# Performance work log

Hardware: AMD Instinct MI355X
Metric: run time of the kernel (lower is better)

## Reference

```python
import jax, jax.numpy as jnp
import numpy as np

N, E = 50000, 800000
IN_DIM, HIDDEN, LATENT = 128, 256, 64


def setup_inputs() -> dict:
    key = jax.random.key(0)
    ks = jax.random.split(key, 10)
    def lin(k, fan_in, fan_out):
        s = 1.0 / np.sqrt(fan_in)
        return jax.random.uniform(k, (fan_in, fan_out), jnp.float32, -s, s)
    x = jax.random.normal(ks[0], (N, IN_DIM), jnp.float32)
    edge_index = jax.random.randint(ks[1], (2, E), 0, N, jnp.int64)
    return {
        "x": x,
        "edge_index": edge_index,
        # enc1: SAGEConv(in_dim, hidden): lin_l (neighbors, with bias), lin_r (root, no bias)
        "W1l": lin(ks[2], IN_DIM, HIDDEN),
        "b1": jnp.zeros((HIDDEN,), jnp.float32),
        "W1r": lin(ks[3], IN_DIM, HIDDEN),
        # enc2: SAGEConv(hidden, latent)
        "W2l": lin(ks[4], HIDDEN, LATENT),
        "b2": jnp.zeros((LATENT,), jnp.float32),
        "W2r": lin(ks[5], HIDDEN, LATENT),
        # decoder Linear(latent, in_dim)
        "Wd": lin(ks[6], LATENT, IN_DIM),
        "bd": jax.random.uniform(ks[7], (IN_DIM,), jnp.float32, -1.0 / np.sqrt(LATENT), 1.0 / np.sqrt(LATENT)),
    }


def _sage_conv(x, src, dst, Wl, b, Wr, num_nodes):
    # PyG SAGEConv (aggr='mean'): out = lin_l(mean_{j in N(i)} x_j) + lin_r(x_i)
    summed = jax.ops.segment_sum(x[src], dst, num_segments=num_nodes)   # [N, d]
    cnt = jax.ops.segment_sum(jnp.ones((src.shape[0],), x.dtype), dst, num_segments=num_nodes)
    mean = summed / jnp.maximum(cnt, 1.0)[:, None]
    return mean @ Wl + b + x @ Wr


def reference(x, edge_index, W1l, b1, W1r, W2l, b2, W2r, Wd, bd):
    src, dst = edge_index[0], edge_index[1]
    n = x.shape[0]
    h = jax.nn.relu(_sage_conv(x, src, dst, W1l, b1, W1r, n))
    z = _sage_conv(h, src, dst, W2l, b2, W2r, n)
    x_hat = z @ Wd + bd
    return (z, x_hat)
```

## Files before the change

kernel.cpp:

```cpp
#include <hip/hip_runtime.h>
#include <stdint.h>

#define NN 50000
#define NE 800000
#define NB 196
#define NBK 196
#define NBUK 196
#define CHK 4096
#define MTOT (NBUK * NBK)
#define MSB 151
#define CVTB 6250
#define PREPB 418

typedef __bf16 bf16x8 __attribute__((ext_vector_type(8)));
typedef float f32x4 __attribute__((ext_vector_type(4)));
typedef unsigned short ushort_t;

__device__ inline float bf2f(uint16_t u) {
    union { uint32_t i; float f; } v; v.i = ((uint32_t)u) << 16; return v.f;
}
__device__ inline uint16_t f2bf(float f) {
    uint32_t u = __float_as_uint(f);
    u += 0x7fffu + ((u >> 16) & 1u);
    return (uint16_t)(u >> 16);
}
__device__ inline float rdf(const void* p, int i, int bf) {
    return bf ? bf2f(((const ushort_t*)p)[i]) : ((const float*)p)[i];
}

__device__ inline int blk_or(int v, int* flag) {
    if (threadIdx.x == 0) *flag = 0;
    __syncthreads();
    if (v) atomicOr(flag, 1);
    __syncthreads();
    return *flag;
}
__device__ inline int detect_sh(const int* __restrict__ ei, int* flag) {
    int t = threadIdx.x;
    int v = ei[2 * t + 1] | ei[2 * (t + 256) + 1] | ei[2 * (t + 512) + 1] | ei[2 * (t + 768) + 1];
    return blk_or(v, flag) ? 0 : 1;
}
__device__ inline int detect_bf(const ushort_t* __restrict__ xw, int* flag) {
    int t = threadIdx.x;
    int bad = 0;
#pragma unroll
    for (int r = 0; r < 2; ++r) {
        uint16_t w = xw[t + 256 * r];
        int e = (w >> 7) & 0xFF;
        if (!(w == 0 || (e >= 96 && e <= 144))) bad = 1;
    }
    return blk_or(bad, flag) ? 0 : 1;
}

__global__ __launch_bounds__(256) void k_stage1(const int* __restrict__ ei, const void* __restrict__ x,
                                                const void* __restrict__ W1l, const void* __restrict__ W1r,
                                                const void* __restrict__ W2l, const void* __restrict__ W2r,
                                                const void* __restrict__ Wd,
                                                const void* __restrict__ b1, const void* __restrict__ b2,
                                                const void* __restrict__ bd,
                                                int* __restrict__ cntm, ushort_t* __restrict__ xb,
                                                ushort_t* __restrict__ wt, ushort_t* __restrict__ w2lt,
                                                ushort_t* __restrict__ w2rt, ushort_t* __restrict__ wdt,
                                                float* __restrict__ b1f, float* __restrict__ b2f,
                                                float* __restrict__ bdf) {
    __shared__ int flag;
    int b = blockIdx.x, t = threadIdx.x;
    if (b < NBK) {
        int sh = detect_sh(ei, &flag);
        __shared__ int hist[NBUK];
        if (t < NBUK) hist[t] = 0;
        __syncthreads();
        for (int i = t; i < CHK; i += 256) {
            int e = b * CHK + i;
            if (e < NE) {
                int d = ei[(size_t)(NE + e) << sh];
                atomicAdd(&hist[d >> 8], 1);
            }
        }
        __syncthreads();
        if (t < NBUK) cntm[t * NBK + b] = hist[t];
    } else if (b < NBK + CVTB) {
        int bf = detect_bf((const ushort_t*)x, &flag);
        int i = (b - NBK) * 256 + t;
        if (bf) {
            reinterpret_cast<ushort4*>(xb)[i] = reinterpret_cast<const ushort4*>(x)[i];
        } else {
            float4 v = reinterpret_cast<const float4*>(x)[i];
            ushort4 o;
            o.x = f2bf(v.x); o.y = f2bf(v.y); o.z = f2bf(v.z); o.w = f2bf(v.w);
            reinterpret_cast<ushort4*>(xb)[i] = o;
        }
    } else {
        int bf = detect_bf((const ushort_t*)x, &flag);
        int idx = (b - NBK - CVTB) * 256 + t;
        if (idx < 65536) {
            int c = idx >> 8, k = idx & 255;
            float v = (k < 128) ? rdf(W1l, k * 256 + c, bf) : rdf(W1r, (k - 128) * 256 + c, bf);
            wt[c * 256 + k] = f2bf(v);
        } else if (idx < 81920) {
            int t2 = idx - 65536;
            int c = t2 >> 8, k = t2 & 255;
            w2lt[c * 256 + k] = f2bf(rdf(W2l, k * 64 + c, bf));
        } else if (idx < 98304) {
            int t2 = idx - 81920;
            int c = t2 >> 8, k = t2 & 255;
            w2rt[c * 256 + k] = f2bf(rdf(W2r, k * 64 + c, bf));
        } else if (idx < 106496) {
            int t2 = idx - 98304;
            int c = t2 >> 6, k = t2 & 63;
            wdt[c * 64 + k] = f2bf(rdf(Wd, k * 128 + c, bf));
        } else if (idx < 106752) {
            b1f[idx - 106496] = rdf(b1, idx - 106496, bf);
        } else if (idx < 106816) {
            b2f[idx - 106752] = rdf(b2, idx - 106752, bf);
        } else if (idx < 106944) {
            bdf[idx - 106816] = rdf(bd, idx - 106816, bf);
        }
    }
}

__device__ inline int block_scan256(int v, int* ws, int* btot) {
    int lane = threadIdx.x & 63, wv = threadIdx.x >> 6;
    int incl = v;
#pragma unroll
    for (int d = 1; d < 64; d <<= 1) {
        int n = __shfl_up(incl, d);
        if (lane >= d) incl += n;
    }
    if (lane == 63) ws[wv] = incl;
    __syncthreads();
    if (threadIdx.x == 0) {
        int r = 0;
#pragma unroll
        for (int k = 0; k < 4; ++k) { int t = ws[k]; ws[k] = r; r += t; }
        *btot = r;
    }
    __syncthreads();
    return ws[wv] + incl - v;
}

__global__ __launch_bounds__(256) void k_scanMA(const int* __restrict__ cntm, int* __restrict__ offm,
                                                int* __restrict__ bsM) {
    __shared__ int ws[4]; __shared__ int btot;
    int i = blockIdx.x * 256 + threadIdx.x;
    int v = (i < MTOT) ? cntm[i] : 0;
    int excl = block_scan256(v, ws, &btot);
    if (i < MTOT) offm[i] = excl;
    if (threadIdx.x == 0) bsM[blockIdx.x] = btot;
}

__global__ __launch_bounds__(256) void k_scanMC2(int* __restrict__ offm, const int* __restrict__ bsM) {
    __shared__ int red[256];
    int t = threadIdx.x, b = blockIdx.x;
    red[t] = (t < b) ? bsM[t] : 0;
    __syncthreads();
#pragma unroll
    for (int s = 128; s > 0; s >>= 1) {
        if (t < s) red[t] += red[t + s];
        __syncthreads();
    }
    int boff = red[0];
    int i = b * 256 + t;
    if (i < MTOT) offm[i] += boff;
}

__global__ __launch_bounds__(256) void k_scatterC(const int* __restrict__ ei,
                                                  const int* __restrict__ offm, uint32_t* __restrict__ pairs) {
    __shared__ int cur[NBUK];
    __shared__ int flag;
    int t = threadIdx.x, blk = blockIdx.x;
    int sh = detect_sh(ei, &flag);
    if (t < NBUK) cur[t] = offm[t * NBK + blk];
    __syncthreads();
    for (int i = t; i < CHK; i += 256) {
        int e = blk * CHK + i;
        if (e < NE) {
            int s = ei[(size_t)e << sh];
            int d = ei[(size_t)(NE + e) << sh];
            int pos = atomicAdd(&cur[d >> 8], 1);
            pairs[pos] = (uint32_t)s | ((uint32_t)(d & 255) << 16);
        }
    }
}

__global__ __launch_bounds__(256) void k_d1s(const uint32_t* __restrict__ pairs, const int* __restrict__ offm,
                                             int* __restrict__ rowptr, int* __restrict__ blocksum) {
    __shared__ int hist[256];
    __shared__ int ws[4]; __shared__ int btot;
    int t = threadIdx.x, b = blockIdx.x;
    hist[t] = 0;
    __syncthreads();
    int beg = offm[b * NBK];
    int end = (b + 1 < NBUK) ? offm[(b + 1) * NBK] : NE;
    for (int i = beg + t; i < end; i += 256) {
        uint32_t p = pairs[i];
        atomicAdd(&hist[p >> 16], 1);
    }
    __syncthreads();
    int v = hist[t];
    int excl = block_scan256(v, ws, &btot);
    int node = b * 256 + t;
    if (node < NN) rowptr[node] = excl;
    if (t == 0) blocksum[b] = btot;
}

__global__ __launch_bounds__(256) void k_scanC2(int* __restrict__ rowptr, const int* __restrict__ blocksum) {
    __shared__ int red[256];
    int t = threadIdx.x, b = blockIdx.x;
    red[t] = (t < b && t < NB) ? blocksum[t] : 0;
    __syncthreads();
#pragma unroll
    for (int s = 128; s > 0; s >>= 1) {
        if (t < s) red[t] += red[t + s];
        __syncthreads();
    }
    int boff = red[0];
    int i = b * 256 + t;
    if (i < NN) rowptr[i] += boff;
    if (b == 0 && t == 0) rowptr[NN] = NE;
}

__global__ __launch_bounds__(256) void k_d2(const uint32_t* __restrict__ pairs, const int* __restrict__ offm,
                                            const int* __restrict__ rowptr, ushort_t* __restrict__ srclist) {
    __shared__ int cur[256];
    int t = threadIdx.x, b = blockIdx.x;
    int node = b * 256 + t;
    cur[t] = (node < NN) ? rowptr[node] : 0;
    __syncthreads();
    int beg = offm[b * NBK];
    int end = (b + 1 < NBUK) ? offm[(b + 1) * NBK] : NE;
    for (int i = beg + t; i < end; i += 256) {
        uint32_t p = pairs[i];
        int pos = atomicAdd(&cur[p >> 16], 1);
        srclist[pos] = (ushort_t)(p & 0xffff);
    }
}

__global__ __launch_bounds__(256) void k_agg128(const ushort_t* __restrict__ xb, const int* __restrict__ rowptr,
                                                const ushort_t* __restrict__ srclist, ushort_t* __restrict__ out) {
    int node = (blockIdx.x * 256 + threadIdx.x) >> 6;
    int lane = threadIdx.x & 63;
    if (node >= NN) return;
    int beg = rowptr[node], end = rowptr[node + 1];
    float a0 = 0.f, a1 = 0.f;
    int j = beg;
    for (; j + 7 < end; j += 8) {
        uint32_t p[8];
#pragma unroll
        for (int u = 0; u < 8; ++u) {
            int s = srclist[j + u];
            p[u] = *reinterpret_cast<const uint32_t*>(xb + (size_t)s * 128 + lane * 2);
        }
#pragma unroll
        for (int u = 0; u < 8; ++u) {
            a0 += bf2f((uint16_t)(p[u] & 0xffff));
            a1 += bf2f((uint16_t)(p[u] >> 16));
        }
    }
    for (; j + 3 < end; j += 4) {
        uint32_t p[4];
#pragma unroll
        for (int u = 0; u < 4; ++u) {
            int s = srclist[j + u];
            p[u] = *reinterpret_cast<const uint32_t*>(xb + (size_t)s * 128 + lane * 2);
        }
#pragma unroll
        for (int u = 0; u < 4; ++u) {
            a0 += bf2f((uint16_t)(p[u] & 0xffff));
            a1 += bf2f((uint16_t)(p[u] >> 16));
        }
    }
    for (; j < end; ++j) {
        int s = srclist[j];
        uint32_t p = *reinterpret_cast<const uint32_t*>(xb + (size_t)s * 128 + lane * 2);
        a0 += bf2f((uint16_t)(p & 0xffff));
        a1 += bf2f((uint16_t)(p >> 16));
    }
    float inv = 1.0f / (float)max(end - beg, 1);
    uint32_t o = (uint32_t)f2bf(a0 * inv) | ((uint32_t)f2bf(a1 * inv) << 16);
    *reinterpret_cast<uint32_t*>(out + (size_t)node * 128 + lane * 2) = o;
}

__global__ __launch_bounds__(256, 2) void k_gemm1p(const ushort_t* __restrict__ meanx, const ushort_t* __restrict__ xb,
                                                   const ushort_t* __restrict__ wt, const float* __restrict__ b1f,
                                                   ushort_t* __restrict__ h) {
    int wv = threadIdx.x >> 6, lane = threadIdx.x & 63;
    int m = lane & 15, q = lane >> 4;
    bf16x8 B[8][4];
#pragma unroll
    for (int ks = 0; ks < 8; ++ks) {
        int kb = ks * 32 + q * 8;
#pragma unroll
        for (int ct = 0; ct < 4; ++ct)
            B[ks][ct] = *reinterpret_cast<const bf16x8*>(wt + (size_t)(wv * 64 + ct * 16 + m) * 256 + kb);
    }
    const int ntiles = NN / 16;
    for (int t = blockIdx.x; t < ntiles; t += gridDim.x) {
        int r0 = t * 16;
        int row = r0 + m;
        f32x4 acc[4];
#pragma unroll
        for (int ct = 0; ct < 4; ++ct) acc[ct] = (f32x4){0.f, 0.f, 0.f, 0.f};
#pragma unroll
        for (int ks = 0; ks < 8; ++ks) {
            int kb = ks * 32 + q * 8;
            const ushort_t* ap = (ks < 4) ? (meanx + (size_t)row * 128 + kb)
                                          : (xb + (size_t)row * 128 + (kb - 128));
            bf16x8 a = *reinterpret_cast<const bf16x8*>(ap);
#pragma unroll
            for (int ct = 0; ct < 4; ++ct)
                acc[ct] = __builtin_amdgcn_mfma_f32_16x16x32_bf16(a, B[ks][ct], acc[ct], 0, 0, 0);
        }
#pragma unroll
        for (int ct = 0; ct < 4; ++ct) {
            int c = wv * 64 + ct * 16 + m;
            float bias = b1f[c];
#pragma unroll
            for (int i = 0; i < 4; ++i) {
                int rr = r0 + q * 4 + i;
                h[(size_t)rr * 256 + c] = f2bf(fmaxf(acc[ct][i] + bias, 0.f));
            }
        }
    }
}

__global__ __launch_bounds__(256, 2) void k_gemm2p(const ushort_t* __restrict__ h,
                                                   const ushort_t* __restrict__ w2lt, const ushort_t* __restrict__ w2rt,
                                                   const float* __restrict__ b2f,
                                                   ushort_t* __restrict__ y, float* __restrict__ r) {
    int wv = threadIdx.x >> 6, lane = threadIdx.x & 63;
    int m = lane & 15, q = lane >> 4;
    int op = wv >> 1;
    int cb = (wv & 1) * 32;
    const ushort_t* wtx = op ? w2rt : w2lt;
    bf16x8 B[8][2];
#pragma unroll
    for (int ks = 0; ks < 8; ++ks) {
        int kb = ks * 32 + q * 8;
#pragma unroll
        for (int ct = 0; ct < 2; ++ct)
            B[ks][ct] = *reinterpret_cast<const bf16x8*>(wtx + (size_t)(cb + ct * 16 + m) * 256 + kb);
    }
    const int ntiles = NN / 16;
    for (int t = blockIdx.x; t < ntiles; t += gridDim.x) {
        int r0 = t * 16;
        int row = r0 + m;
        f32x4 acc[2];
        acc[0] = (f32x4){0.f, 0.f, 0.f, 0.f}; acc[1] = acc[0];
#pragma unroll
        for (int ks = 0; ks < 8; ++ks) {
            int kb = ks * 32 + q * 8;
            bf16x8 a = *reinterpret_cast<const bf16x8*>(h + (size_t)row * 256 + kb);
#pragma unroll
            for (int ct = 0; ct < 2; ++ct)
                acc[ct] = __builtin_amdgcn_mfma_f32_16x16x32_bf16(a, B[ks][ct], acc[ct], 0, 0, 0);
        }
#pragma unroll
        for (int ct = 0; ct < 2; ++ct) {
            int c = cb + ct * 16 + m;
#pragma unroll
            for (int i = 0; i < 4; ++i) {
                int rr = r0 + q * 4 + i;
                if (op == 0) y[(size_t)rr * 64 + c] = f2bf(acc[ct][i]);
                else         r[(size_t)rr * 64 + c] = acc[ct][i] + b2f[c];
            }
        }
    }
}

__global__ __launch_bounds__(256) void k_agg2g3(const ushort_t* __restrict__ y, const int* __restrict__ rowptr,
                                                const ushort_t* __restrict__ srclist,
                                                float* zr,
                                                const ushort_t* __restrict__ wdt, const float* __restrict__ bdf,
                                                float* __restrict__ xhat) {
    __shared__ alignas(16) ushort_t zt[16][72];
    int b = blockIdx.x;
    int wv = threadIdx.x >> 6, lane = threadIdx.x & 63;
    int m = lane & 15, q = lane >> 4;
    bf16x8 B[2][2];
#pragma unroll
    for (int ks = 0; ks < 2; ++ks) {
        int kb = ks * 32 + q * 8;
#pragma unroll
        for (int ct = 0; ct < 2; ++ct)
            B[ks][ct] = *reinterpret_cast<const bf16x8*>(wdt + (size_t)(wv * 32 + ct * 16 + m) * 64 + kb);
    }
    float bias0 = bdf[wv * 32 + m], bias1 = bdf[wv * 32 + 16 + m];

    int half = lane >> 5, l32 = lane & 31;
#pragma unroll
    for (int s = 0; s < 4; ++s) {
        int node = b * 16 + wv * 4 + s;
        int beg = rowptr[node], end = rowptr[node + 1];
        float a0 = 0.f, a1 = 0.f;
        int j = beg + half;
        for (; j + 6 < end; j += 8) {
            uint32_t p[4];
#pragma unroll
            for (int u = 0; u < 4; ++u) {
                int sx = srclist[j + 2 * u];
                p[u] = *reinterpret_cast<const uint32_t*>(y + (size_t)sx * 64 + l32 * 2);
            }
#pragma unroll
            for (int u = 0; u < 4; ++u) {
                a0 += bf2f((uint16_t)(p[u] & 0xffff));
                a1 += bf2f((uint16_t)(p[u] >> 16));
            }
        }
        for (; j < end; j += 2) {
            int sx = srclist[j];
            uint32_t p = *reinterpret_cast<const uint32_t*>(y + (size_t)sx * 64 + l32 * 2);
            a0 += bf2f((uint16_t)(p & 0xffff));
            a1 += bf2f((uint16_t)(p >> 16));
        }
        a0 += __shfl_xor(a0, 32);
        a1 += __shfl_xor(a1, 32);
        if (half == 0) {
            float inv = 1.0f / (float)max(end - beg, 1);
            float2 rv = *reinterpret_cast<const float2*>(zr + (size_t)node * 64 + l32 * 2);
            float z0 = a0 * inv + rv.x;
            float z1 = a1 * inv + rv.y;
            float2 zo; zo.x = z0; zo.y = z1;
            *reinterpret_cast<float2*>(zr + (size_t)node * 64 + l32 * 2) = zo;
            uint32_t o = (uint32_t)f2bf(z0) | ((uint32_t)f2bf(z1) << 16);
            *reinterpret_cast<uint32_t*>(&zt[wv * 4 + s][l32 * 2]) = o;
        }
    }
    __syncthreads();
    f32x4 acc[2];
    acc[0] = (f32x4){0.f, 0.f, 0.f, 0.f}; acc[1] = acc[0];
#pragma unroll
    for (int ks = 0; ks < 2; ++ks) {
        bf16x8 a = *reinterpret_cast<const bf16x8*>(&zt[m][ks * 32 + q * 8]);
#pragma unroll
        for (int ct = 0; ct < 2; ++ct)
            acc[ct] = __builtin_amdgcn_mfma_f32_16x16x32_bf16(a, B[ks][ct], acc[ct], 0, 0, 0);
    }
#pragma unroll
    for (int ct = 0; ct < 2; ++ct) {
        int c = wv * 32 + ct * 16 + m;
        float bb = ct ? bias1 : bias0;
#pragma unroll
        for (int i = 0; i < 4; ++i) {
            int rr = b * 16 + q * 4 + i;
            xhat[(size_t)rr * 128 + c] = acc[ct][i] + bb;
        }
    }
}

extern "C" void kernel_launch(void* const* d_in, const int* in_sizes, int n_in,
                              void* d_out, int out_size, void* d_ws, size_t ws_size,
                              hipStream_t stream) {
    const void *px = nullptr, *pei = nullptr, *pW1l = nullptr, *pW1r = nullptr,
               *pW2l = nullptr, *pW2r = nullptr, *pWd = nullptr,
               *pb1 = nullptr, *pb2 = nullptr, *pbd = nullptr;
    for (int i = 0; i < n_in; ++i) {
        const void* p = d_in[i];
        switch (in_sizes[i]) {
            case 6400000: px  = p; break;
            case 1600000: pei = p; break;
            case 32768:   if (!pW1l) pW1l = p; else pW1r = p; break;
            case 16384:   if (!pW2l) pW2l = p; else pW2r = p; break;
            case 8192:    pWd = p; break;
            case 256:     pb1 = p; break;
            case 128:     pbd = p; break;
            case 64:      pb2 = p; break;
            default: break;
        }
    }
    if (!px || !pei || !pW1l || !pW1r || !pW2l || !pW2r || !pWd || !pb1 || !pb2 || !pbd) {
        px = d_in[0]; pei = d_in[1]; pW1l = d_in[2]; pb1 = d_in[3]; pW1r = d_in[4];
        pW2l = d_in[5]; pb2 = d_in[6]; pW2r = d_in[7]; pWd = d_in[8]; pbd = d_in[9];
    }
    const int* ei = (const int*)pei;

    char* base = (char*)d_ws;
    size_t off = 0;
    auto alloc = [&](size_t bytes) -> void* {
        void* r = base + off;
        off = (off + bytes + 255) & ~(size_t)255;
        return r;
    };
    int* rowptr   = (int*)alloc((size_t)(NN + 1) * 4);
    int* blocksum = (int*)alloc((size_t)NB * 4);
    int* cntm     = (int*)alloc((size_t)MTOT * 4);
    int* offm     = (int*)alloc((size_t)MTOT * 4);
    int* bsM      = (int*)alloc(256 * 4);
    ushort_t* srclist = (ushort_t*)alloc((size_t)NE * 2);
    ushort_t* wt   = (ushort_t*)alloc((size_t)65536 * 2);
    ushort_t* w2lt = (ushort_t*)alloc((size_t)16384 * 2);
    ushort_t* w2rt = (ushort_t*)alloc((size_t)16384 * 2);
    ushort_t* wdt  = (ushort_t*)alloc((size_t)8192 * 2);
    float* b1f    = (float*)alloc(256 * 4);
    float* b2f    = (float*)alloc(64 * 4);
    float* bdf    = (float*)alloc(128 * 4);
    ushort_t* xb  = (ushort_t*)alloc((size_t)NN * 128 * 2);
    ushort_t* h   = (ushort_t*)alloc((size_t)NN * 256 * 2);

    uint32_t* pairs = (uint32_t*)h;

    float* out_z    = (float*)d_out;
    float* out_xhat = out_z + (size_t)NN * 64;

    ushort_t* meanx = (ushort_t*)out_xhat;
    ushort_t* y     = xb;
    float*    rbuf  = out_z;

    k_stage1<<<NBK + CVTB + PREPB, 256, 0, stream>>>(ei, px, pW1l, pW1r, pW2l, pW2r, pWd, pb1, pb2, pbd,
                                                     cntm, xb, wt, w2lt, w2rt, wdt, b1f, b2f, bdf);

    k_scanMA<<<MSB, 256, 0, stream>>>(cntm, offm, bsM);
    k_scanMC2<<<MSB, 256, 0, stream>>>(offm, bsM);
    k_scatterC<<<NBK, 256, 0, stream>>>(ei, offm, pairs);
    k_d1s<<<NBUK, 256, 0, stream>>>(pairs, offm, rowptr, blocksum);
    k_scanC2<<<NB, 256, 0, stream>>>(rowptr, blocksum);
    k_d2<<<NBUK, 256, 0, stream>>>(pairs, offm, rowptr, srclist);

    int ab = (NN + 3) / 4;
    k_agg128<<<ab, 256, 0, stream>>>(xb, rowptr, srclist, meanx);

    k_gemm1p<<<512, 256, 0, stream>>>(meanx, xb, wt, b1f, h);
    k_gemm2p<<<512, 256, 0, stream>>>(h, w2lt, w2rt, b2f, y, rbuf);
    k_agg2g3<<<NN / 16, 256, 0, stream>>>(y, rowptr, srclist, rbuf, wdt, bdf, out_xhat);
}
```

Measured before the change: 248.9 us.

## Build CSR with global atomics and fuse layer-1 and layer-2 GEMMs via LDS

Replaces the two-level bucketed counting sort (bucket histograms, matrix scan, pair scatter, per-bucket local sort) with a per-node global atomic histogram, a two-pass scan, and a direct atomic scatter into the source list. This cuts several kernel launches and the intermediate pairs buffer. It also fuses the layer-1 GEMM with the layer-2 projection: each 16-row hidden tile is written to swizzled shared memory and consumed immediately, so the hidden matrix never goes to global memory. The costs are heavier global atomic contention, non-deterministic edge order within each row, extra register pressure from holding both weight sets, and more per-tile synchronisation.

```diff
diff --git a/kernel.cpp b/kernel.cpp
--- a/kernel.cpp
+++ b/kernel.cpp
@@ -5,12 +5,10 @@
 #define NE 800000
 #define NB 196
 #define NBK 196
-#define NBUK 196
 #define CHK 4096
-#define MTOT (NBUK * NBK)
-#define MSB 151
 #define CVTB 6250
 #define PREPB 418
+#define CURN (NB * 256)
 
 typedef __bf16 bf16x8 __attribute__((ext_vector_type(8)));
 typedef float f32x4 __attribute__((ext_vector_type(4)));
@@ -58,7 +56,7 @@
                                                 const void* __restrict__ Wd,
                                                 const void* __restrict__ b1, const void* __restrict__ b2,
                                                 const void* __restrict__ bd,
-                                                int* __restrict__ cntm, ushort_t* __restrict__ xb,
+                                                int* __restrict__ cur, ushort_t* __restrict__ xb,
                                                 ushort_t* __restrict__ wt, ushort_t* __restrict__ w2lt,
                                                 ushort_t* __restrict__ w2rt, ushort_t* __restrict__ wdt,
                                                 float* __restrict__ b1f, float* __restrict__ b2f,
@@ -67,18 +65,13 @@
     int b = blockIdx.x, t = threadIdx.x;
     if (b < NBK) {
         int sh = detect_sh(ei, &flag);
-        __shared__ int hist[NBUK];
-        if (t < NBUK) hist[t] = 0;
-        __syncthreads();
         for (int i = t; i < CHK; i += 256) {
             int e = b * CHK + i;
             if (e < NE) {
                 int d = ei[(size_t)(NE + e) << sh];
-                atomicAdd(&hist[d >> 8], 1);
+                atomicAdd(&cur[d], 1);
             }
         }
-        __syncthreads();
-        if (t < NBUK) cntm[t * NBK + b] = hist[t];
     } else if (b < NBK + CVTB) {
         int bf = detect_bf((const ushort_t*)x, &flag);
         int i = (b - NBK) * 256 + t;
@@ -139,20 +132,21 @@
     return ws[wv] + incl - v;
 }
 
-__global__ __launch_bounds__(256) void k_scanMA(const int* __restrict__ cntm, int* __restrict__ offm,
-                                                int* __restrict__ bsM) {
+__global__ __launch_bounds__(256) void k_scanA(const int* __restrict__ cur, int* __restrict__ rowptr,
+                                               int* __restrict__ blocksum) {
     __shared__ int ws[4]; __shared__ int btot;
     int i = blockIdx.x * 256 + threadIdx.x;
-    int v = (i < MTOT) ? cntm[i] : 0;
+    int v = (i < NN) ? cur[i] : 0;
     int excl = block_scan256(v, ws, &btot);
-    if (i < MTOT) offm[i] = excl;
-    if (threadIdx.x == 0) bsM[blockIdx.x] = btot;
-}
-
-__global__ __launch_bounds__(256) void k_scanMC2(int* __restrict__ offm, const int* __restrict__ bsM) {
+    if (i < NN) rowptr[i] = excl;
+    if (threadIdx.x == 0) blocksum[blockIdx.x] = btot;
+}
+
+__global__ __launch_bounds__(256) void k_scanfix(int* __restrict__ rowptr, const int* __restrict__ blocksum,
+                                                 int* __restrict__ cur) {
     __shared__ int red[256];
     int t = threadIdx.x, b = blockIdx.x;
-    red[t] = (t < b) ? bsM[t] : 0;
+    red[t] = (t < b && t < NB) ? blocksum[t] : 0;
     __syncthreads();
 #pragma unroll
     for (int s = 128; s > 0; s >>= 1) {
@@ -161,78 +155,27 @@
     }
     int boff = red[0];
     int i = b * 256 + t;
-    if (i < MTOT) offm[i] += boff;
-}
-
-__global__ __launch_bounds__(256) void k_scatterC(const int* __restrict__ ei,
-                                                  const int* __restrict__ offm, uint32_t* __restrict__ pairs) {
-    __shared__ int cur[NBUK];
+    if (i < NN) {
+        int v = rowptr[i] + boff;
+        rowptr[i] = v;
+        cur[i] = v;
+    }
+    if (b == 0 && t == 0) rowptr[NN] = NE;
+}
+
+__global__ __launch_bounds__(256) void k_scatter(const int* __restrict__ ei, int* __restrict__ cur,
+                                                 ushort_t* __restrict__ srclist) {
     __shared__ int flag;
     int t = threadIdx.x, blk = blockIdx.x;
     int sh = detect_sh(ei, &flag);
-    if (t < NBUK) cur[t] = offm[t * NBK + blk];
-    __syncthreads();
     for (int i = t; i < CHK; i += 256) {
         int e = blk * CHK + i;
         if (e < NE) {
             int s = ei[(size_t)e << sh];
             int d = ei[(size_t)(NE + e) << sh];
-            int pos = atomicAdd(&cur[d >> 8], 1);
-            pairs[pos] = (uint32_t)s | ((uint32_t)(d & 255) << 16);
-        }
-    }
-}
-
-__global__ __launch_bounds__(256) void k_d1s(const uint32_t* __restrict__ pairs, const int* __restrict__ offm,
-                                             int* __restrict__ rowptr, int* __restrict__ blocksum) {
-    __shared__ int hist[256];
-    __shared__ int ws[4]; __shared__ int btot;
-    int t = threadIdx.x, b = blockIdx.x;
-    hist[t] = 0;
-    __syncthreads();
-    int beg = offm[b * NBK];
-    int end = (b + 1 < NBUK) ? offm[(b + 1) * NBK] : NE;
-    for (int i = beg + t; i < end; i += 256) {
-        uint32_t p = pairs[i];
-        atomicAdd(&hist[p >> 16], 1);
-    }
-    __syncthreads();
-    int v = hist[t];
-    int excl = block_scan256(v, ws, &btot);
-    int node = b * 256 + t;
-    if (node < NN) rowptr[node] = excl;
-    if (t == 0) blocksum[b] = btot;
-}
-
-__global__ __launch_bounds__(256) void k_scanC2(int* __restrict__ rowptr, const int* __restrict__ blocksum) {
-    __shared__ int red[256];
-    int t = threadIdx.x, b = blockIdx.x;
-    red[t] = (t < b && t < NB) ? blocksum[t] : 0;
-    __syncthreads();
-#pragma unroll
-    for (int s = 128; s > 0; s >>= 1) {
-        if (t < s) red[t] += red[t + s];
-        __syncthreads();
-    }
-    int boff = red[0];
-    int i = b * 256 + t;
-    if (i < NN) rowptr[i] += boff;
-    if (b == 0 && t == 0) rowptr[NN] = NE;
-}
-
-__global__ __launch_bounds__(256) void k_d2(const uint32_t* __restrict__ pairs, const int* __restrict__ offm,
-                                            const int* __restrict__ rowptr, ushort_t* __restrict__ srclist) {
-    __shared__ int cur[256];
-    int t = threadIdx.x, b = blockIdx.x;
-    int node = b * 256 + t;
-    cur[t] = (node < NN) ? rowptr[node] : 0;
-    __syncthreads();
-    int beg = offm[b * NBK];
-    int end = (b + 1 < NBUK) ? offm[(b + 1) * NBK] : NE;
-    for (int i = beg + t; i < end; i += 256) {
-        uint32_t p = pairs[i];
-        int pos = atomicAdd(&cur[p >> 16], 1);
-        srclist[pos] = (ushort_t)(p & 0xffff);
+            int pos = atomicAdd(&cur[d], 1);
+            srclist[pos] = (ushort_t)s;
+        }
     }
 }
 
@@ -281,19 +224,37 @@
     *reinterpret_cast<uint32_t*>(out + (size_t)node * 128 + lane * 2) = o;
 }
 
-__global__ __launch_bounds__(256, 2) void k_gemm1p(const ushort_t* __restrict__ meanx, const ushort_t* __restrict__ xb,
+__global__ __launch_bounds__(256, 2) void k_gemm12(const ushort_t* __restrict__ meanx, const ushort_t* __restrict__ xb,
                                                    const ushort_t* __restrict__ wt, const float* __restrict__ b1f,
-                                                   ushort_t* __restrict__ h) {
+                                                   const ushort_t* __restrict__ w2lt, const ushort_t* __restrict__ w2rt,
+                                                   const float* __restrict__ b2f,
+                                                   ushort_t* __restrict__ y, float* __restrict__ r) {
+    __shared__ alignas(16) ushort_t ht[16 * 256];
     int wv = threadIdx.x >> 6, lane = threadIdx.x & 63;
     int m = lane & 15, q = lane >> 4;
-    bf16x8 B[8][4];
+    bf16x8 B1[8][4];
 #pragma unroll
     for (int ks = 0; ks < 8; ++ks) {
         int kb = ks * 32 + q * 8;
 #pragma unroll
         for (int ct = 0; ct < 4; ++ct)
-            B[ks][ct] = *reinterpret_cast<const bf16x8*>(wt + (size_t)(wv * 64 + ct * 16 + m) * 256 + kb);
-    }
+            B1[ks][ct] = *reinterpret_cast<const bf16x8*>(wt + (size_t)(wv * 64 + ct * 16 + m) * 256 + kb);
+    }
+    int op = wv >> 1;
+    int cb = (wv & 1) * 32;
+    const ushort_t* wtx = op ? w2rt : w2lt;
+    bf16x8 B2[8][2];
+#pragma unroll
+    for (int ks = 0; ks < 8; ++ks) {
+        int kb = ks * 32 + q * 8;
+#pragma unroll
+        for (int ct = 0; ct < 2; ++ct)
+            B2[ks][ct] = *reinterpret_cast<const bf16x8*>(wtx + (size_t)(cb + ct * 16 + m) * 256 + kb);
+    }
+    float bias2[2];
+#pragma unroll
+    for (int ct = 0; ct < 2; ++ct) bias2[ct] = b2f[cb + ct * 16 + m];
+
     const int ntiles = NN / 16;
     for (int t = blockIdx.x; t < ntiles; t += gridDim.x) {
         int r0 = t * 16;
@@ -309,7 +270,7 @@
             bf16x8 a = *reinterpret_cast<const bf16x8*>(ap);
 #pragma unroll
             for (int ct = 0; ct < 4; ++ct)
-                acc[ct] = __builtin_amdgcn_mfma_f32_16x16x32_bf16(a, B[ks][ct], acc[ct], 0, 0, 0);
+                acc[ct] = __builtin_amdgcn_mfma_f32_16x16x32_bf16(a, B1[ks][ct], acc[ct], 0, 0, 0);
         }
 #pragma unroll
         for (int ct = 0; ct < 4; ++ct) {
@@ -317,43 +278,22 @@
             float bias = b1f[c];
 #pragma unroll
             for (int i = 0; i < 4; ++i) {
-                int rr = r0 + q * 4 + i;
-                h[(size_t)rr * 256 + c] = f2bf(fmaxf(acc[ct][i] + bias, 0.f));
+                int lr = q * 4 + i;
+                int off = (lr * 512 + c * 2) ^ ((lr & 7) << 4);
+                *reinterpret_cast<ushort_t*>(reinterpret_cast<char*>(ht) + off) =
+                    f2bf(fmaxf(acc[ct][i] + bias, 0.f));
             }
         }
-    }
-}
-
-__global__ __launch_bounds__(256, 2) void k_gemm2p(const ushort_t* __restrict__ h,
-                                                   const ushort_t* __restrict__ w2lt, const ushort_t* __restrict__ w2rt,
-                                                   const float* __restrict__ b2f,
-                                                   ushort_t* __restrict__ y, float* __restrict__ r) {
-    int wv = threadIdx.x >> 6, lane = threadIdx.x & 63;
-    int m = lane & 15, q = lane >> 4;
-    int op = wv >> 1;
-    int cb = (wv & 1) * 32;
-    const ushort_t* wtx = op ? w2rt : w2lt;
-    bf16x8 B[8][2];
-#pragma unroll
-    for (int ks = 0; ks < 8; ++ks) {
-        int kb = ks * 32 + q * 8;
-#pragma unroll
-        for (int ct = 0; ct < 2; ++ct)
-            B[ks][ct] = *reinterpret_cast<const bf16x8*>(wtx + (size_t)(cb + ct * 16 + m) * 256 + kb);
-    }
-    const int ntiles = NN / 16;
-    for (int t = blockIdx.x; t < ntiles; t += gridDim.x) {
-        int r0 = t * 16;
-        int row = r0 + m;
-        f32x4 acc[2];
-        acc[0] = (f32x4){0.f, 0.f, 0.f, 0.f}; acc[1] = acc[0];
+        __syncthreads();
+        f32x4 acc2[2];
+        acc2[0] = (f32x4){0.f, 0.f, 0.f, 0.f}; acc2[1] = acc2[0];
 #pragma unroll
         for (int ks = 0; ks < 8; ++ks) {
-            int kb = ks * 32 + q * 8;
-            bf16x8 a = *reinterpret_cast<const bf16x8*>(h + (size_t)row * 256 + kb);
+            int boff = (m * 512 + ks * 64 + q * 16) ^ ((m & 7) << 4);
+            bf16x8 a = *reinterpret_cast<const bf16x8*>(reinterpret_cast<const char*>(ht) + boff);
 #pragma unroll
             for (int ct = 0; ct < 2; ++ct)
-                acc[ct] = __builtin_amdgcn_mfma_f32_16x16x32_bf16(a, B[ks][ct], acc[ct], 0, 0, 0);
+                acc2[ct] = __builtin_amdgcn_mfma_f32_16x16x32_bf16(a, B2[ks][ct], acc2[ct], 0, 0, 0);
         }
 #pragma unroll
         for (int ct = 0; ct < 2; ++ct) {
@@ -361,10 +301,11 @@
 #pragma unroll
             for (int i = 0; i < 4; ++i) {
                 int rr = r0 + q * 4 + i;
-                if (op == 0) y[(size_t)rr * 64 + c] = f2bf(acc[ct][i]);
-                else         r[(size_t)rr * 64 + c] = acc[ct][i] + b2f[c];
+                if (op == 0) y[(size_t)rr * 64 + c] = f2bf(acc2[ct][i]);
+                else         r[(size_t)rr * 64 + c] = acc2[ct][i] + bias2[ct];
             }
         }
+        __syncthreads();
     }
 }
 
@@ -483,9 +424,7 @@
     };
     int* rowptr   = (int*)alloc((size_t)(NN + 1) * 4);
     int* blocksum = (int*)alloc((size_t)NB * 4);
-    int* cntm     = (int*)alloc((size_t)MTOT * 4);
-    int* offm     = (int*)alloc((size_t)MTOT * 4);
-    int* bsM      = (int*)alloc(256 * 4);
+    int* cur      = (int*)alloc((size_t)CURN * 4);
     ushort_t* srclist = (ushort_t*)alloc((size_t)NE * 2);
     ushort_t* wt   = (ushort_t*)alloc((size_t)65536 * 2);
     ushort_t* w2lt = (ushort_t*)alloc((size_t)16384 * 2);
@@ -495,31 +434,26 @@
     float* b2f    = (float*)alloc(64 * 4);
     float* bdf    = (float*)alloc(128 * 4);
     ushort_t* xb  = (ushort_t*)alloc((size_t)NN * 128 * 2);
-    ushort_t* h   = (ushort_t*)alloc((size_t)NN * 256 * 2);
-
-    uint32_t* pairs = (uint32_t*)h;
+    ushort_t* y   = (ushort_t*)alloc((size_t)NN * 64 * 2);
 
     float* out_z    = (float*)d_out;
     float* out_xhat = out_z + (size_t)NN * 64;
 
     ushort_t* meanx = (ushort_t*)out_xhat;
-    ushort_t* y     = xb;
     float*    rbuf  = out_z;
 
+    hipMemsetAsync(cur, 0, (size_t)CURN * 4, stream);
+
     k_stage1<<<NBK + CVTB + PREPB, 256, 0, stream>>>(ei, px, pW1l, pW1r, pW2l, pW2r, pWd, pb1, pb2, pbd,
-                                                     cntm, xb, wt, w2lt, w2rt, wdt, b1f, b2f, bdf);
-
-    k_scanMA<<<MSB, 256, 0, stream>>>(cntm, offm, bsM);
-    k_scanMC2<<<MSB, 256, 0, stream>>>(offm, bsM);
-    k_scatterC<<<NBK, 256, 0, stream>>>(ei, offm, pairs);
-    k_d1s<<<NBUK, 256, 0, stream>>>(pairs, offm, rowptr, blocksum);
-    k_scanC2<<<NB, 256, 0, stream>>>(rowptr, blocksum);
-    k_d2<<<NBUK, 256, 0, stream>>>(pairs, offm, rowptr, srclist);
+                                                     cur, xb, wt, w2lt, w2rt, wdt, b1f, b2f, bdf);
+
+    k_scanA<<<NB, 256, 0, stream>>>(cur, rowptr, blocksum);
+    k_scanfix<<<NB, 256, 0, stream>>>(rowptr, blocksum, cur);
+    k_scatter<<<NBK, 256, 0, stream>>>(ei, cur, srclist);
 
     int ab = (NN + 3) / 4;
     k_agg128<<<ab, 256, 0, stream>>>(xb, rowptr, srclist, meanx);
 
-    k_gemm1p<<<512, 256, 0, stream>>>(meanx, xb, wt, b1f, h);
-    k_gemm2p<<<512, 256, 0, stream>>>(h, w2lt, w2rt, b2f, y, rbuf);
+    k_gemm12<<<512, 256, 0, stream>>>(meanx, xb, wt, b1f, w2lt, w2rt, b2f, y, rbuf);
     k_agg2g3<<<NN / 16, 256, 0, stream>>>(y, rowptr, srclist, rbuf, wdt, bdf, out_xhat);
 }
```

After: 271.3 us. 9.0% more time.

## Fuse layer-1 and layer-2 GEMMs via swizzled LDS tile of h

Applied to the files above, without the earlier changes.

Merges the first SAGE GEMM (with ReLU) and the second-layer projection GEMM into one kernel. Each 16-row tile of the hidden activation h is written to XOR-swizzled shared memory and consumed there, so the 50000x256 bf16 h buffer is never written to or read back from global memory, and one launch is dropped. In exchange it adds two block barriers per tile, keeps both weight sets in registers (more register pressure, which may lower occupancy), and gives pairs and y their own workspace buffers instead of aliasing h and xb.

```diff
diff --git a/kernel.cpp b/kernel.cpp
--- a/kernel.cpp
+++ b/kernel.cpp
@@ -281,19 +281,37 @@
     *reinterpret_cast<uint32_t*>(out + (size_t)node * 128 + lane * 2) = o;
 }
 
-__global__ __launch_bounds__(256, 2) void k_gemm1p(const ushort_t* __restrict__ meanx, const ushort_t* __restrict__ xb,
+__global__ __launch_bounds__(256, 2) void k_gemm12(const ushort_t* __restrict__ meanx, const ushort_t* __restrict__ xb,
                                                    const ushort_t* __restrict__ wt, const float* __restrict__ b1f,
-                                                   ushort_t* __restrict__ h) {
+                                                   const ushort_t* __restrict__ w2lt, const ushort_t* __restrict__ w2rt,
+                                                   const float* __restrict__ b2f,
+                                                   ushort_t* __restrict__ y, float* __restrict__ r) {
+    __shared__ alignas(16) ushort_t ht[16 * 256];
     int wv = threadIdx.x >> 6, lane = threadIdx.x & 63;
     int m = lane & 15, q = lane >> 4;
-    bf16x8 B[8][4];
+    bf16x8 B1[8][4];
 #pragma unroll
     for (int ks = 0; ks < 8; ++ks) {
         int kb = ks * 32 + q * 8;
 #pragma unroll
         for (int ct = 0; ct < 4; ++ct)
-            B[ks][ct] = *reinterpret_cast<const bf16x8*>(wt + (size_t)(wv * 64 + ct * 16 + m) * 256 + kb);
-    }
+            B1[ks][ct] = *reinterpret_cast<const bf16x8*>(wt + (size_t)(wv * 64 + ct * 16 + m) * 256 + kb);
+    }
+    int op = wv >> 1;
+    int cb = (wv & 1) * 32;
+    const ushort_t* wtx = op ? w2rt : w2lt;
+    bf16x8 B2[8][2];
+#pragma unroll
+    for (int ks = 0; ks < 8; ++ks) {
+        int kb = ks * 32 + q * 8;
+#pragma unroll
+        for (int ct = 0; ct < 2; ++ct)
+            B2[ks][ct] = *reinterpret_cast<const bf16x8*>(wtx + (size_t)(cb + ct * 16 + m) * 256 + kb);
+    }
+    float bias2[2];
+#pragma unroll
+    for (int ct = 0; ct < 2; ++ct) bias2[ct] = b2f[cb + ct * 16 + m];
+
     const int ntiles = NN / 16;
     for (int t = blockIdx.x; t < ntiles; t += gridDim.x) {
         int r0 = t * 16;
@@ -309,7 +327,7 @@
             bf16x8 a = *reinterpret_cast<const bf16x8*>(ap);
 #pragma unroll
             for (int ct = 0; ct < 4; ++ct)
-                acc[ct] = __builtin_amdgcn_mfma_f32_16x16x32_bf16(a, B[ks][ct], acc[ct], 0, 0, 0);
+                acc[ct] = __builtin_amdgcn_mfma_f32_16x16x32_bf16(a, B1[ks][ct], acc[ct], 0, 0, 0);
         }
 #pragma unroll
         for (int ct = 0; ct < 4; ++ct) {
@@ -317,43 +335,22 @@
             float bias = b1f[c];
 #pragma unroll
             for (int i = 0; i < 4; ++i) {
-                int rr = r0 + q * 4 + i;
-                h[(size_t)rr * 256 + c] = f2bf(fmaxf(acc[ct][i] + bias, 0.f));
+                int lr = q * 4 + i;
+                int off = (lr * 512 + c * 2) ^ ((lr & 7) << 4);
+                *reinterpret_cast<ushort_t*>(reinterpret_cast<char*>(ht) + off) =
+                    f2bf(fmaxf(acc[ct][i] + bias, 0.f));
             }
         }
-    }
-}
-
-__global__ __launch_bounds__(256, 2) void k_gemm2p(const ushort_t* __restrict__ h,
-                                                   const ushort_t* __restrict__ w2lt, const ushort_t* __restrict__ w2rt,
-                                                   const float* __restrict__ b2f,
-                                                   ushort_t* __restrict__ y, float* __restrict__ r) {
-    int wv = threadIdx.x >> 6, lane = threadIdx.x & 63;
-    int m = lane & 15, q = lane >> 4;
-    int op = wv >> 1;
-    int cb = (wv & 1) * 32;
-    const ushort_t* wtx = op ? w2rt : w2lt;
-    bf16x8 B[8][2];
-#pragma unroll
-    for (int ks = 0; ks < 8; ++ks) {
-        int kb = ks * 32 + q * 8;
-#pragma unroll
-        for (int ct = 0; ct < 2; ++ct)
-            B[ks][ct] = *reinterpret_cast<const bf16x8*>(wtx + (size_t)(cb + ct * 16 + m) * 256 + kb);
-    }
-    const int ntiles = NN / 16;
-    for (int t = blockIdx.x; t < ntiles; t += gridDim.x) {
-        int r0 = t * 16;
-        int row = r0 + m;
-        f32x4 acc[2];
-        acc[0] = (f32x4){0.f, 0.f, 0.f, 0.f}; acc[1] = acc[0];
+        __syncthreads();
+        f32x4 acc2[2];
+        acc2[0] = (f32x4){0.f, 0.f, 0.f, 0.f}; acc2[1] = acc2[0];
 #pragma unroll
         for (int ks = 0; ks < 8; ++ks) {
-            int kb = ks * 32 + q * 8;
-            bf16x8 a = *reinterpret_cast<const bf16x8*>(h + (size_t)row * 256 + kb);
+            int boff = (m * 512 + ks * 64 + q * 16) ^ ((m & 7) << 4);
+            bf16x8 a = *reinterpret_cast<const bf16x8*>(reinterpret_cast<const char*>(ht) + boff);
 #pragma unroll
             for (int ct = 0; ct < 2; ++ct)
-                acc[ct] = __builtin_amdgcn_mfma_f32_16x16x32_bf16(a, B[ks][ct], acc[ct], 0, 0, 0);
+                acc2[ct] = __builtin_amdgcn_mfma_f32_16x16x32_bf16(a, B2[ks][ct], acc2[ct], 0, 0, 0);
         }
 #pragma unroll
         for (int ct = 0; ct < 2; ++ct) {
@@ -361,10 +358,11 @@
 #pragma unroll
             for (int i = 0; i < 4; ++i) {
                 int rr = r0 + q * 4 + i;
-                if (op == 0) y[(size_t)rr * 64 + c] = f2bf(acc[ct][i]);
-                else         r[(size_t)rr * 64 + c] = acc[ct][i] + b2f[c];
+                if (op == 0) y[(size_t)rr * 64 + c] = f2bf(acc2[ct][i]);
+                else         r[(size_t)rr * 64 + c] = acc2[ct][i] + bias2[ct];
             }
         }
+        __syncthreads();
     }
 }
 
@@ -486,6 +484,7 @@
     int* cntm     = (int*)alloc((size_t)MTOT * 4);
     int* offm     = (int*)alloc((size_t)MTOT * 4);
     int* bsM      = (int*)alloc(256 * 4);
+    uint32_t* pairs = (uint32_t*)alloc((size_t)NE * 4);
     ushort_t* srclist = (ushort_t*)alloc((size_t)NE * 2);
     ushort_t* wt   = (ushort_t*)alloc((size_t)65536 * 2);
     ushort_t* w2lt = (ushort_t*)alloc((size_t)16384 * 2);
@@ -495,15 +494,12 @@
     float* b2f    = (float*)alloc(64 * 4);
     float* bdf    = (float*)alloc(128 * 4);
     ushort_t* xb  = (ushort_t*)alloc((size_t)NN * 128 * 2);
-    ushort_t* h   = (ushort_t*)alloc((size_t)NN * 256 * 2);
-
-    uint32_t* pairs = (uint32_t*)h;
+    ushort_t* y   = (ushort_t*)alloc((size_t)NN * 64 * 2);
 
     float* out_z    = (float*)d_out;
     float* out_xhat = out_z + (size_t)NN * 64;
 
     ushort_t* meanx = (ushort_t*)out_xhat;
-    ushort_t* y     = xb;
     float*    rbuf  = out_z;
 
     k_stage1<<<NBK + CVTB + PREPB, 256, 0, stream>>>(ei, px, pW1l, pW1r, pW2l, pW2r, pWd, pb1, pb2, pbd,
@@ -519,7 +515,6 @@
     int ab = (NN + 3) / 4;
     k_agg128<<<ab, 256, 0, stream>>>(xb, rowptr, srclist, meanx);
 
-    k_gemm1p<<<512, 256, 0, stream>>>(meanx, xb, wt, b1f, h);
-    k_gemm2p<<<512, 256, 0, stream>>>(h, w2lt, w2rt, b2f, y, rbuf);
+    k_gemm12<<<512, 256, 0, stream>>>(meanx, xb, wt, b1f, w2lt, w2rt, b2f, y, rbuf);
     k_agg2g3<<<NN / 16, 256, 0, stream>>>(y, rowptr, srclist, rbuf, wdt, bdf, out_xhat);
 }
```

Result: faster. 230.6 us (-7.3%).
